# Optimization experiments

Measured on AMD Instinct MI355X. Metric: run time of the kernel, lower is better.

Reference implementation:

```python
import jax, jax.numpy as jnp
import numpy as np

BETA = 0.25
CODEBOOK_SIZE = 4096
DIM = 512


def setup_inputs() -> dict:
    key = jax.random.key(0)
    k1, k2 = jax.random.split(key)
    z_e = jax.random.normal(k1, (16, 1024, 512), dtype=jnp.float32)
    # kaiming_uniform-ish codebook init
    bound = float(np.sqrt(6.0 / ((1.0 + 5.0) * DIM)))
    embed = jax.random.uniform(k2, (CODEBOOK_SIZE, DIM), dtype=jnp.float32,
                               minval=-bound, maxval=bound)
    return {"z_e": z_e, "embed": embed}


def reference(z_e, embed):
    D = embed.shape[1]
    K = embed.shape[0]
    z = z_e.reshape(-1, D)                                   # [N, D]
    N = z.shape[0]
    # squared euclidean distances [N, K]
    distances = (jnp.sum(z * z, axis=1, keepdims=True)
                 - 2.0 * (z @ embed.T)
                 + jnp.sum(embed * embed, axis=1))
    indices = jnp.argmin(distances, axis=1)                  # [N]
    z_q = embed[indices].reshape(z_e.shape)                  # gather == one-hot matmul
    # straight-through estimator
    z_q_st = z_e + jax.lax.stop_gradient(z_q - z_e)
    commitment_loss = jnp.mean((jax.lax.stop_gradient(z_q) - z_e) ** 2)
    vq_loss = BETA * commitment_loss
    # avg_probs = encodings.mean(0) via histogram of indices
    counts = jnp.zeros((K,), dtype=z.dtype).at[indices].add(1.0)
    avg_probs = counts / N
    perplexity = jnp.exp(-jnp.sum(avg_probs * jnp.log(avg_probs + 1e-10)))
    return (z_q_st, indices.reshape(z_e.shape[:-1]), vq_loss, perplexity)
```

## Files before the change

kernel.cpp:

```cpp
#include <hip/hip_runtime.h>
#include <cstdint>
#include <cstddef>

typedef _Float16 f16x8 __attribute__((ext_vector_type(8)));
typedef float f32x4 __attribute__((ext_vector_type(4)));

#define NTOK 16384
#define DIMV 512
#define KCODE 4096

#define IDX_OFF (NTOK * DIMV)
#define LOSSO   (IDX_OFF + NTOK)
#define PERPO   (LOSSO + 1)

static const size_t A2_OFF = 0;
static const size_t B2_OFF = A2_OFF + (size_t)NTOK * DIMV * 2;
static const size_t EN_OFF = B2_OFF + (size_t)KCODE * DIMV * 2;
static const size_t RK_OFF = EN_OFF + (size_t)KCODE * 4;
static const size_t CNT_OFF = RK_OFF + (size_t)NTOK * 32 * 4;
static const size_t RLOSS_OFF = CNT_OFF + (size_t)KCODE * 4;

__device__ __forceinline__ float sqf(float v) {
    float p = v * v;
    asm volatile("" : "+v"(p));
    return p;
}

__device__ __forceinline__ float np_pairwise_sq(const float* xs, int t) {
    float accp = 0.0f;
    if (t < 32) {
        const float* blk = xs + (t >> 3) * 128;
        int j = t & 7;
        float rj = sqf(blk[j]);
#pragma unroll
        for (int tt = 1; tt < 16; ++tt) rj += sqf(blk[tt * 8 + j]);
        accp = rj;
    }
#pragma unroll
    for (int d = 1; d <= 16; d <<= 1) accp += __shfl_xor(accp, d, 64);
    return __shfl(accp, 0, 64);
}

__global__ void prep_k(const float* __restrict__ z, const float* __restrict__ e,
                       _Float16* __restrict__ A2, _Float16* __restrict__ B2,
                       float* __restrict__ C32, unsigned* __restrict__ counts) {
    __shared__ float es[4][512];
    const int b = blockIdx.x;
    if (b < 4096) {
        int t = b * 256 + threadIdx.x;
        int n = t >> 6;
        int dc = (t & 63) << 3;
        const float* zp = z + (size_t)n * DIMV + dc;
        float4 v0 = ((const float4*)zp)[0];
        float4 v1 = ((const float4*)zp)[1];
        float vs[8] = {v0.x, v0.y, v0.z, v0.w, v1.x, v1.y, v1.z, v1.w};
        f16x8 hi;
#pragma unroll
        for (int i = 0; i < 8; ++i) hi[i] = (_Float16)(vs[i] * 256.0f);
        *(f16x8*)(A2 + (size_t)n * DIMV + dc) = hi;
    } else {
        const int wv = threadIdx.x >> 6, t = threadIdx.x & 63;
        const int k = (b - 4096) * 4 + wv;
        const float* ep = e + (size_t)k * DIMV + t * 8;
        float4 v0 = ((const float4*)ep)[0];
        float4 v1 = ((const float4*)ep)[1];
        ((float4*)es[wv])[t * 2] = v0;
        ((float4*)es[wv])[t * 2 + 1] = v1;
        float vs[8] = {v0.x, v0.y, v0.z, v0.w, v1.x, v1.y, v1.z, v1.w};
        f16x8 hi;
#pragma unroll
        for (int i = 0; i < 8; ++i) hi[i] = (_Float16)(vs[i] * 256.0f);
        *(f16x8*)(B2 + (size_t)k * DIMV + t * 8) = hi;
        float c = np_pairwise_sq(es[wv], t);
        if (t == 0) C32[k] = c;
        if (threadIdx.x < 4) counts[(b - 4096) * 4 + threadIdx.x] = 0u;
    }
}

typedef uint32_t __attribute__((address_space(1))) gas_u32;
typedef uint32_t __attribute__((address_space(3))) las_u32;
__device__ __forceinline__ void g2l16(const _Float16* g, _Float16* l) {
    __builtin_amdgcn_global_load_lds((const gas_u32*)(uintptr_t)g,
                                     (las_u32*)(uint32_t)(uintptr_t)l, 16, 0, 0);
}

__device__ __forceinline__ void top2_merge32(unsigned& k1, unsigned& k2,
                                             unsigned o1, unsigned o2) {
    unsigned n1 = k1 < o1 ? k1 : o1;
    unsigned mx = k1 < o1 ? o1 : k1;
    unsigned n2 = k2 < o2 ? k2 : o2;
    k1 = n1;
    k2 = mx < n2 ? mx : n2;
}

#define DPP_TOP2(CTRL)                                                                     \
    {                                                                                      \
        unsigned o1 = (unsigned)__builtin_amdgcn_update_dpp(-1, (int)k1, CTRL, 0xF, 0xF, false); \
        unsigned o2 = (unsigned)__builtin_amdgcn_update_dpp(-1, (int)k2, CTRL, 0xF, 0xF, false); \
        top2_merge32(k1, k2, o1, o2);                                                      \
    }

#define PHASE(MH, KS, LOADB, STAGE_CALL)                                           \
    {                                                                              \
        f16x8 af[4];                                                               \
        _Pragma("unroll") for (int i = 0; i < 4; ++i)                              \
            af[i] = *(const f16x8*)&L[bb + (KS)*8192 + aOff + ((MH)*4 + i) * 512]; \
        if (LOADB) {                                                               \
            _Pragma("unroll") for (int j = 0; j < 4; ++j)                          \
                bf[j] = *(const f16x8*)&L[bb + (KS)*8192 + bOff + j * 512];        \
        }                                                                          \
        STAGE_CALL;                                                                \
        __builtin_amdgcn_s_setprio(1);                                             \
        _Pragma("unroll") for (int i = 0; i < 4; ++i)                              \
            _Pragma("unroll") for (int j = 0; j < 4; ++j)                          \
                acc[(MH)*4 + i][j] = __builtin_amdgcn_mfma_f32_16x16x32_f16(       \
                    af[i], bf[j], acc[(MH)*4 + i][j], 0, 0, 0);                    \
        __builtin_amdgcn_s_setprio(0);                                             \
    }

__global__ __launch_bounds__(512, 2) void gemm_top2_k(
    const _Float16* __restrict__ A2, const _Float16* __restrict__ B2,
    const float* __restrict__ C32, unsigned* __restrict__ rk2) {
    __shared__ __align__(16) _Float16 L[65536];

    const int nt = blockIdx.x;
    const int mt = blockIdx.y;
    const int tid = threadIdx.x;
    const int w = tid >> 6, l = tid & 63;
    const int wm = w >> 2, wn = w & 3;
    const int lane15 = l & 15, q = l >> 4;

    const int lo = l >> 2;
    const int cswz = (l & 3) ^ ((l >> 3) & 3);
    const _Float16* aSrc0 = A2 + (size_t)(mt * 256 + w * 16 + lo) * DIMV + cswz * 8;
    const _Float16* aSrc1 = A2 + (size_t)(mt * 256 + 128 + w * 16 + lo) * DIMV + cswz * 8;
    const _Float16* bSrc0 = B2 + (size_t)(nt * 256 + w * 16 + lo) * DIMV + cswz * 8;
    const _Float16* bSrc1 = B2 + (size_t)(nt * 256 + 128 + w * 16 + lo) * DIMV + cswz * 8;

    auto stageA = [&](int nb_, int kh, int kt) {
        g2l16(aSrc0 + kt * 64 + kh * 32, &L[nb_ + kh * 8192 + w * 512]);
        g2l16(aSrc1 + kt * 64 + kh * 32, &L[nb_ + kh * 8192 + 4096 + w * 512]);
    };
    auto stageB = [&](int nb_, int kh, int kt) {
        g2l16(bSrc0 + kt * 64 + kh * 32, &L[nb_ + 16384 + kh * 8192 + w * 512]);
        g2l16(bSrc1 + kt * 64 + kh * 32, &L[nb_ + 16384 + kh * 8192 + 4096 + w * 512]);
    };

    const int slot8 = (q ^ ((lane15 >> 1) & 3)) * 8;
    const int aOff = (wm * 128 + lane15) * 32 + slot8;
    const int bOff = 16384 + (wn * 64 + lane15) * 32 + slot8;

    f32x4 acc[8][4] = {};
    f16x8 bf[4];

    stageA(0, 0, 0); stageB(0, 0, 0); stageA(0, 1, 0); stageB(0, 1, 0);

    for (int t = 0; t < 8; ++t) {
        const int bb = (t & 1) << 15;
        const int nb = ((t + 1) & 1) << 15;
        const bool pf = t < 7;
        asm volatile("s_waitcnt vmcnt(4)" ::: "memory");
        __builtin_amdgcn_s_barrier();
        PHASE(0, 0, true, if (pf) stageA(nb, 0, t + 1))
        __builtin_amdgcn_s_barrier();
        PHASE(1, 0, false, if (pf) stageB(nb, 0, t + 1))
        if (pf) { asm volatile("s_waitcnt vmcnt(4)" ::: "memory"); }
        else    { asm volatile("s_waitcnt vmcnt(0)" ::: "memory"); }
        __builtin_amdgcn_s_barrier();
        PHASE(0, 1, true, if (pf) stageA(nb, 1, t + 1))
        __builtin_amdgcn_s_barrier();
        PHASE(1, 1, false, if (pf) stageB(nb, 1, t + 1))
    }
    __builtin_amdgcn_s_barrier();

    unsigned* lk32 = (unsigned*)L;
    const int colL = wn * 64 + lane15;
    float envals[4];
#pragma unroll
    for (int j = 0; j < 4; ++j) envals[j] = C32[nt * 256 + colL + j * 16] * 65536.0f + 4.0e6f;

#pragma unroll
    for (int mf = 0; mf < 8; ++mf) {
#pragma unroll
        for (int rr = 0; rr < 4; ++rr) {
            unsigned k1 = 0xFFFFFFFFu, k2 = 0xFFFFFFFFu;
#pragma unroll
            for (int j = 0; j < 4; ++j) {
                float dist = envals[j] - 2.0f * acc[mf][j][rr];
                unsigned key = (__float_as_uint(dist) & 0xFFFFFF00u) | (unsigned)(colL + j * 16);
                if (key < k1) { k2 = k1; k1 = key; } else if (key < k2) k2 = key;
            }
            DPP_TOP2(0x118)
            DPP_TOP2(0x114)
            DPP_TOP2(0x112)
            DPP_TOP2(0x111)
            if (lane15 == 15) {
                int rl = wm * 128 + mf * 16 + q * 4 + rr;
                lk32[rl * 10 + wn * 2]     = k1;
                lk32[rl * 10 + wn * 2 + 1] = k2;
            }
        }
    }
    __syncthreads();
    if (tid < 256) {
        unsigned a1 = lk32[tid * 10], a2 = lk32[tid * 10 + 1];
#pragma unroll
        for (int p = 1; p < 4; ++p)
            top2_merge32(a1, a2, lk32[tid * 10 + p * 2], lk32[tid * 10 + p * 2 + 1]);
        size_t base = (size_t)(mt * 256 + tid) * 32 + nt * 2;
        rk2[base] = a1;
        rk2[base + 1] = a2;
    }
}

__global__ __launch_bounds__(256) void refine_k(
    const unsigned* __restrict__ rk2,
    const float* __restrict__ embed, const float* __restrict__ z,
    const float* __restrict__ C32,
    float* __restrict__ out, unsigned* __restrict__ counts,
    double* __restrict__ rloss) {
    __shared__ float zs[4][512];
    __shared__ float zqs[4][512];
    const int wv = threadIdx.x >> 6, t = threadIdx.x & 63;
    const int r = blockIdx.x * 4 + wv;
    const float4* zp = (const float4*)(z + (size_t)r * DIMV);
    float4 za = zp[t * 2], zb = zp[t * 2 + 1];
    ((float4*)zs[wv])[t * 2] = za;
    ((float4*)zs[wv])[t * 2 + 1] = zb;
    __syncthreads();

    float A32 = np_pairwise_sq(zs[wv], t);

    unsigned long long key = ~0ull;
    if (t < 32) {
        unsigned kraw = rk2[(size_t)r * 32 + t];
        unsigned col = (unsigned)(t >> 1) * 256u + (kraw & 255u);
        key = ((unsigned long long)(kraw & 0xFFFFFF00u) << 32) | col;
    }

    const int g = t >> 4, j = t & 15;
    unsigned mycand = 0;
#pragma unroll
    for (int c = 0; c < 4; ++c) {
        unsigned long long m = key;
#pragma unroll
        for (int d = 1; d < 64; d <<= 1) {
            unsigned long long o = __shfl_xor(m, d, 64);
            m = o < m ? o : m;
        }
        if (c == g) mycand = (unsigned)(m & 0xFFFFFFFFull);
        if (key == m) key = ~0ull;
    }

    const float4* ep = (const float4*)(embed + (size_t)mycand * DIMV);
    float4 ev[8];
    double s = 0.0;
#pragma unroll
    for (int it = 0; it < 8; ++it) {
        float4 e4 = ep[j + it * 16];
        ev[it] = e4;
        float4 z4 = ((const float4*)zs[wv])[j + it * 16];
        s += (double)z4.x * e4.x + (double)z4.y * e4.y +
             (double)z4.z * e4.z + (double)z4.w * e4.w;
    }
#pragma unroll
    for (int d = 1; d < 16; d <<= 1) s += __shfl_xor(s, d, 64);

    float Bf = (float)s;
    float d32 = (A32 - 2.0f * Bf) + C32[mycand];
    unsigned u = __float_as_uint(d32);
    u = (u & 0x80000000u) ? ~u : (u | 0x80000000u);
    unsigned long long dk = ((unsigned long long)u << 32) | mycand;
#pragma unroll
    for (int d = 16; d < 64; d <<= 1) {
        unsigned long long o = __shfl_xor(dk, d, 64);
        dk = o < dk ? o : dk;
    }
    const unsigned ibest = (unsigned)(dk & 0xFFFFFFFFull);

    if (mycand == ibest) {
#pragma unroll
        for (int it = 0; it < 8; ++it) ((float4*)zqs[wv])[j + it * 16] = ev[it];
    }
    __syncthreads();

    float4 wa = ((const float4*)zqs[wv])[t * 2];
    float4 wb = ((const float4*)zqs[wv])[t * 2 + 1];
    float4* op = (float4*)(out + (size_t)r * DIMV);
    op[t * 2] = wa;
    op[t * 2 + 1] = wb;
    double dx0 = (double)za.x - wa.x, dx1 = (double)za.y - wa.y;
    double dx2 = (double)za.z - wa.z, dx3 = (double)za.w - wa.w;
    double dx4 = (double)zb.x - wb.x, dx5 = (double)zb.y - wb.y;
    double dx6 = (double)zb.z - wb.z, dx7 = (double)zb.w - wb.w;
    double ls = dx0 * dx0 + dx1 * dx1 + dx2 * dx2 + dx3 * dx3 +
                dx4 * dx4 + dx5 * dx5 + dx6 * dx6 + dx7 * dx7;
#pragma unroll
    for (int d = 1; d < 64; d <<= 1) ls += __shfl_xor(ls, d, 64);
    if (t == 0) {
        out[IDX_OFF + r] = (float)ibest;
        rloss[r] = ls;
        atomicAdd(&counts[ibest], 1u);
    }
}

__global__ __launch_bounds__(1024) void scalars_k(
    const unsigned* __restrict__ counts,
    const double* __restrict__ rloss, float* __restrict__ out) {
    int t = threadIdx.x;
    double ls = 0.0;
    for (int i = t; i < NTOK; i += 1024) ls += rloss[i];
#pragma unroll
    for (int d = 1; d < 64; d <<= 1) ls += __shfl_xor(ls, d, 64);
    float s = 0.0f;
    for (int i = t; i < KCODE; i += 1024) {
        float p = (float)counts[i] * (1.0f / (float)NTOK);
        s += p * logf(p + 1e-10f);
    }
#pragma unroll
    for (int d = 1; d < 64; d <<= 1) s += __shfl_xor(s, d, 64);
    __shared__ float red[16];
    __shared__ double redd[16];
    if ((t & 63) == 0) { red[t >> 6] = s; redd[t >> 6] = ls; }
    __syncthreads();
    if (t == 0) {
        float stot = 0.0f;
        double ltot = 0.0;
#pragma unroll
        for (int i = 0; i < 16; ++i) { stot += red[i]; ltot += redd[i]; }
        out[PERPO] = expf(-stot);
        out[LOSSO] = 0.25f * (float)(ltot * (1.0 / (double)(NTOK * DIMV)));
    }
}

extern "C" void kernel_launch(void* const* d_in, const int* in_sizes, int n_in,
                              void* d_out, int out_size, void* d_ws, size_t ws_size,
                              hipStream_t stream) {
    const float* z     = (const float*)d_in[0];
    const float* embed = (const float*)d_in[1];
    float* out = (float*)d_out;
    char* ws = (char*)d_ws;

    _Float16* A2 = (_Float16*)(ws + A2_OFF);
    _Float16* B2 = (_Float16*)(ws + B2_OFF);
    float* C32 = (float*)(ws + EN_OFF);
    unsigned* rk2 = (unsigned*)(ws + RK_OFF);
    unsigned* counts = (unsigned*)(ws + CNT_OFF);
    double* rloss = (double*)(ws + RLOSS_OFF);

    prep_k<<<5120, 256, 0, stream>>>(z, embed, A2, B2, C32, counts);
    gemm_top2_k<<<dim3(16, 64), 512, 0, stream>>>(A2, B2, C32, rk2);
    refine_k<<<NTOK / 4, 256, 0, stream>>>(rk2, embed, z, C32, out, counts, rloss);
    scalars_k<<<1, 1024, 0, stream>>>(counts, rloss, out);
}
```

Measured before the change: 213.1 us.

## Deepen GEMM LDS pipeline to three half-stages and drop LDS swizzle

Restructures the fp16 GEMM main loop so global-to-LDS loads run one and a half k-steps ahead (three staged half-tiles in flight) instead of one. It reorganizes the LDS layout to place A and B for each k-half contiguously. It also removes the XOR swizzle on LDS slots and moves barriers so each one sits after the prefetch issue and the LDS reads, using explicit lgkmcnt waits and sched_barrier. The aim is to hide global-load latency better and cut barrier stalls. The cost is that removing the swizzle may bring back LDS bank conflicts, and the scheduling becomes more rigid.

```diff
diff --git a/kernel.cpp b/kernel.cpp
--- a/kernel.cpp
+++ b/kernel.cpp
@@ -100,22 +100,28 @@
         top2_merge32(k1, k2, o1, o2);                                                      \
     }
 
-#define PHASE(MH, KS, LOADB, STAGE_CALL)                                           \
-    {                                                                              \
-        f16x8 af[4];                                                               \
-        _Pragma("unroll") for (int i = 0; i < 4; ++i)                              \
-            af[i] = *(const f16x8*)&L[bb + (KS)*8192 + aOff + ((MH)*4 + i) * 512]; \
-        if (LOADB) {                                                               \
-            _Pragma("unroll") for (int j = 0; j < 4; ++j)                          \
-                bf[j] = *(const f16x8*)&L[bb + (KS)*8192 + bOff + j * 512];        \
-        }                                                                          \
-        STAGE_CALL;                                                                \
-        __builtin_amdgcn_s_setprio(1);                                             \
-        _Pragma("unroll") for (int i = 0; i < 4; ++i)                              \
-            _Pragma("unroll") for (int j = 0; j < 4; ++j)                          \
-                acc[(MH)*4 + i][j] = __builtin_amdgcn_mfma_f32_16x16x32_f16(       \
-                    af[i], bf[j], acc[(MH)*4 + i][j], 0, 0, 0);                    \
-        __builtin_amdgcn_s_setprio(0);                                             \
+#define PHASE(MH, KS, LOADB, STAGE, WAIT, BAR2)                                   \
+    {                                                                             \
+        const int sb = bb + (KS)*16384;                                           \
+        f16x8 af[4];                                                              \
+        _Pragma("unroll") for (int i = 0; i < 4; ++i)                             \
+            af[i] = *(const f16x8*)&L[sb + aBase + (MH)*2048 + i * 512];          \
+        if (LOADB) {                                                              \
+            _Pragma("unroll") for (int j = 0; j < 4; ++j)                         \
+                bf[j] = *(const f16x8*)&L[sb + bBase + j * 512];                  \
+        }                                                                         \
+        STAGE;                                                                    \
+        WAIT;                                                                     \
+        __builtin_amdgcn_s_barrier();                                             \
+        asm volatile("s_waitcnt lgkmcnt(0)" ::: "memory");                        \
+        __builtin_amdgcn_sched_barrier(0);                                        \
+        __builtin_amdgcn_s_setprio(1);                                            \
+        _Pragma("unroll") for (int i = 0; i < 4; ++i)                             \
+            _Pragma("unroll") for (int j = 0; j < 4; ++j)                         \
+                acc[(MH)*4 + i][j] = __builtin_amdgcn_mfma_f32_16x16x32_f16(      \
+                    af[i], bf[j], acc[(MH)*4 + i][j], 0, 0, 0);                   \
+        __builtin_amdgcn_s_setprio(0);                                            \
+        if (BAR2) __builtin_amdgcn_s_barrier();                                   \
     }
 
 __global__ __launch_bounds__(512, 2) void gemm_top2_k(
@@ -130,48 +136,55 @@
     const int wm = w >> 2, wn = w & 3;
     const int lane15 = l & 15, q = l >> 4;
 
-    const int lo = l >> 2;
-    const int cswz = (l & 3) ^ ((l >> 3) & 3);
-    const _Float16* aSrc0 = A2 + (size_t)(mt * 256 + w * 16 + lo) * DIMV + cswz * 8;
-    const _Float16* aSrc1 = A2 + (size_t)(mt * 256 + 128 + w * 16 + lo) * DIMV + cswz * 8;
-    const _Float16* bSrc0 = B2 + (size_t)(nt * 256 + w * 16 + lo) * DIMV + cswz * 8;
-    const _Float16* bSrc1 = B2 + (size_t)(nt * 256 + 128 + w * 16 + lo) * DIMV + cswz * 8;
-
-    auto stageA = [&](int nb_, int kh, int kt) {
-        g2l16(aSrc0 + kt * 64 + kh * 32, &L[nb_ + kh * 8192 + w * 512]);
-        g2l16(aSrc1 + kt * 64 + kh * 32, &L[nb_ + kh * 8192 + 4096 + w * 512]);
+    const int lr = l >> 2, lk = (l & 3) * 8;
+    const _Float16* aG = A2 + (size_t)(mt * 256 + w * 32 + lr) * DIMV + lk;
+    const _Float16* bG = B2 + (size_t)(nt * 256 + w * 32 + lr) * DIMV + lk;
+
+    auto stA = [&](int dst, int kt, int ks) {
+        const _Float16* s = aG + kt * 64 + ks * 32;
+        _Float16* d = &L[dst + w * 1024];
+        g2l16(s, d);
+        g2l16(s + 16 * DIMV, d + 512);
     };
-    auto stageB = [&](int nb_, int kh, int kt) {
-        g2l16(bSrc0 + kt * 64 + kh * 32, &L[nb_ + 16384 + kh * 8192 + w * 512]);
-        g2l16(bSrc1 + kt * 64 + kh * 32, &L[nb_ + 16384 + kh * 8192 + 4096 + w * 512]);
+    auto stB = [&](int dst, int kt, int ks) {
+        const _Float16* s = bG + kt * 64 + ks * 32;
+        _Float16* d = &L[dst + w * 1024];
+        g2l16(s, d);
+        g2l16(s + 16 * DIMV, d + 512);
     };
 
-    const int slot8 = (q ^ ((lane15 >> 1) & 3)) * 8;
-    const int aOff = (wm * 128 + lane15) * 32 + slot8;
-    const int bOff = 16384 + (wn * 64 + lane15) * 32 + slot8;
+    const int aBase = (wm * 128 + lane15) * 32 + q * 8;
+    const int bBase = 8192 + (wn * 64 + lane15) * 32 + q * 8;
 
     f32x4 acc[8][4] = {};
     f16x8 bf[4];
 
-    stageA(0, 0, 0); stageB(0, 0, 0); stageA(0, 1, 0); stageB(0, 1, 0);
+    stA(0, 0, 0);          stB(8192, 0, 0);
+    stA(16384, 0, 1);      stB(24576, 0, 1);
+    stA(32768, 1, 0);      stB(32768 + 8192, 1, 0);
+    asm volatile("s_waitcnt vmcnt(8)" ::: "memory");
+    __builtin_amdgcn_s_barrier();
 
     for (int t = 0; t < 8; ++t) {
         const int bb = (t & 1) << 15;
-        const int nb = ((t + 1) & 1) << 15;
-        const bool pf = t < 7;
-        asm volatile("s_waitcnt vmcnt(4)" ::: "memory");
-        __builtin_amdgcn_s_barrier();
-        PHASE(0, 0, true, if (pf) stageA(nb, 0, t + 1))
-        __builtin_amdgcn_s_barrier();
-        PHASE(1, 0, false, if (pf) stageB(nb, 0, t + 1))
-        if (pf) { asm volatile("s_waitcnt vmcnt(4)" ::: "memory"); }
-        else    { asm volatile("s_waitcnt vmcnt(0)" ::: "memory"); }
-        __builtin_amdgcn_s_barrier();
-        PHASE(0, 1, true, if (pf) stageA(nb, 1, t + 1))
-        __builtin_amdgcn_s_barrier();
-        PHASE(1, 1, false, if (pf) stageB(nb, 1, t + 1))
-    }
-    __builtin_amdgcn_s_barrier();
+        const int nb = bb ^ 32768;
+        PHASE(0, 0, true,
+              { if (t < 7) stA(nb + 16384, t + 1, 1); },
+              {}, false)
+        PHASE(1, 0, false,
+              { if (t < 7) stB(nb + 24576, t + 1, 1); },
+              { if (t < 7) { asm volatile("s_waitcnt vmcnt(8)" ::: "memory"); }
+                else       { asm volatile("s_waitcnt vmcnt(0)" ::: "memory"); } },
+              true)
+        PHASE(0, 1, true,
+              { if (t < 6) stA(bb, t + 2, 0); },
+              {}, false)
+        PHASE(1, 1, false,
+              { if (t < 6) stB(bb + 8192, t + 2, 0); },
+              { if (t < 6)      { asm volatile("s_waitcnt vmcnt(8)" ::: "memory"); }
+                else if (t == 6){ asm volatile("s_waitcnt vmcnt(4)" ::: "memory"); } },
+              true)
+    }
 
     unsigned* lk32 = (unsigned*)L;
     const int colL = wn * 64 + lane15;
```

Result: slower. 221.4 us (+3.9%).
